# Kernel tuning notes

Hardware: AMD Instinct MI355X
Metric: run time of the kernel (lower is better)

The kernel has to match this reference:

```python
import jax, jax.numpy as jnp
import numpy as np

N = 200000
F = 64   # input_node_features_size
H = 64   # input_node_hidden_state_size
E = 64   # input_edge_hidden_state_size
DEG = 16
OUT = 128          # output_node_hidden_state_size
HALF = OUT // 2    # 64
IN1 = F + H        # 128 (first_layer=False -> concat)
MID1 = (F + H + HALF) // 2  # 96


def setup_inputs() -> dict:
    key = jax.random.key(0)
    ks = jax.random.split(key, 11)
    s = lambda fan_in: 1.0 / np.sqrt(fan_in)
    return {
        "node_features": jax.random.normal(ks[0], (N, F), jnp.float32),
        "node_hidden": jax.random.normal(ks[1], (N, H), jnp.float32),
        "mailbox": jax.random.normal(ks[2], (N, DEG, E), jnp.float32),
        # net_1: Linear(IN1->MID1), Linear(MID1->HALF)
        "w1a": jax.random.uniform(ks[3], (IN1, MID1), jnp.float32, -s(IN1), s(IN1)),
        "b1a": jax.random.uniform(ks[4], (MID1,), jnp.float32, -s(IN1), s(IN1)),
        "w1b": jax.random.uniform(ks[5], (MID1, HALF), jnp.float32, -s(MID1), s(MID1)),
        "b1b": jax.random.uniform(ks[6], (HALF,), jnp.float32, -s(MID1), s(MID1)),
        # net_2: Linear(E->HALF), Linear(HALF->HALF)
        "w2a": jax.random.uniform(ks[7], (E, HALF), jnp.float32, -s(E), s(E)),
        "b2a": jax.random.uniform(ks[8], (HALF,), jnp.float32, -s(E), s(E)),
        "w2b": jax.random.uniform(ks[9], (HALF, HALF), jnp.float32, -s(HALF), s(HALF)),
        "b2b": jax.random.uniform(ks[10], (HALF,), jnp.float32, -s(HALF), s(HALF)),
    }


def reference(node_features, node_hidden, mailbox,
              w1a, b1a, w1b, b1b, w2a, b2a, w2b, b2b):
    # Branch 1: concat(features, hidden) -> Linear -> ReLU -> Linear -> Tanh
    # (dropout is identity at inference)
    x1 = jnp.concatenate([node_features, node_hidden], axis=1)  # [N, IN1]
    h1 = jax.nn.relu(x1 @ w1a + b1a)                            # [N, MID1]
    r1 = jnp.tanh(h1 @ w1b + b1b)                               # [N, HALF]

    # Branch 2: mailbox sum-aggregate -> Linear -> ReLU -> Linear -> Tanh
    x2 = jnp.sum(mailbox, axis=1)                               # [N, E]
    h2 = jax.nn.relu(x2 @ w2a + b2a)                            # [N, HALF]
    r2 = jnp.tanh(h2 @ w2b + b2b)                               # [N, HALF]

    # Concat + per-row L2 (Frobenius over dim=1) normalize
    r = jnp.concatenate([r1, r2], axis=1)                       # [N, OUT]
    norm = jnp.linalg.norm(r, axis=1, keepdims=True)
    return r / norm
```

## Files before the change

kernel.cpp:

```cpp
#include <hip/hip_runtime.h>

constexpr int NB = 64;
constexpr int THREADS = 256;
constexpr int X1SU = 66;
constexpr int H1SU = 50;
constexpr int X2SU = 35;

constexpr int W1A_OFF = 0;
constexpr int W1B_OFF = 6144;
constexpr int W2A_OFF = 9216;
constexpr int W2B_OFF = 11264;
constexpr int WTOTAL  = 13312;

typedef __fp16 half2_t __attribute__((ext_vector_type(2)));

__device__ __forceinline__ float fast_tanh(float x) {
    float e = __expf(2.0f * x);
    return 1.0f - 2.0f * __builtin_amdgcn_rcpf(e + 1.0f);
}

__device__ __forceinline__ unsigned pk16(float a, float b) {
    half2_t h = __builtin_amdgcn_cvt_pkrtz(a, b);
    return __builtin_bit_cast(unsigned, h);
}

__device__ __forceinline__ half2_t uh(unsigned u) {
    return __builtin_bit_cast(half2_t, u);
}

__device__ __forceinline__ void dot24(half2_t pa, half2_t pb,
                                      const unsigned* __restrict__ w0,
                                      const unsigned* __restrict__ w1,
                                      float* __restrict__ acc) {
    #pragma unroll
    for (int j = 0; j < 24; ++j) acc[j] = __builtin_amdgcn_fdot2(pa, uh(w0[j]), acc[j], false);
    #pragma unroll
    for (int j = 0; j < 24; ++j) acc[j] = __builtin_amdgcn_fdot2(pb, uh(w1[j]), acc[j], false);
}

__device__ __forceinline__ void dot16(half2_t pa, half2_t pb,
                                      const unsigned* __restrict__ w0,
                                      const unsigned* __restrict__ w1,
                                      float* __restrict__ acc) {
    #pragma unroll
    for (int j = 0; j < 16; ++j) acc[j] = __builtin_amdgcn_fdot2(pa, uh(w0[j]), acc[j], false);
    #pragma unroll
    for (int j = 0; j < 16; ++j) acc[j] = __builtin_amdgcn_fdot2(pb, uh(w1[j]), acc[j], false);
}

__global__ __launch_bounds__(256) void cvt_weights(
    const float* __restrict__ w1a, const float* __restrict__ w1b,
    const float* __restrict__ w2a, const float* __restrict__ w2b,
    unsigned* __restrict__ wp)
{
    int idx = blockIdx.x * 256 + threadIdx.x;
    const float* src; int cols, rel;
    if (idx < W1B_OFF)      { rel = idx;           src = w1a; cols = 96; }
    else if (idx < W2A_OFF) { rel = idx - W1B_OFF; src = w1b; cols = 64; }
    else if (idx < W2B_OFF) { rel = idx - W2A_OFF; src = w2a; cols = 64; }
    else                    { rel = idx - W2B_OFF; src = w2b; cols = 64; }
    int k2 = rel / cols, j = rel - k2 * cols;
    wp[idx] = pk16(src[(2 * k2) * cols + j], src[(2 * k2 + 1) * cols + j]);
}

__global__ __launch_bounds__(THREADS) void node_net_kernel(
    const float* __restrict__ feat, const float* __restrict__ hid,
    const float* __restrict__ mail,
    const float* __restrict__ b1a, const float* __restrict__ b1b,
    const float* __restrict__ b2a, const float* __restrict__ b2b,
    const unsigned* __restrict__ wp,
    float* __restrict__ out)
{
    __shared__ unsigned ldsA[NB * X1SU];
    __shared__ unsigned ldsB[NB * X2SU];
    __shared__ float    ldsS[NB * 4];

    const int t  = threadIdx.x;
    const int n0 = blockIdx.x * NB;
    const int c4 = t & 15;
    const int nb = t >> 4;

    const float4* mb0 = reinterpret_cast<const float4*>(mail) + (size_t)(n0 + nb) * 256 + c4;

    #pragma unroll
    for (int i = 0; i < 4; ++i) {
        int n = nb + 16 * i;
        float4 f = reinterpret_cast<const float4*>(feat)[(size_t)(n0 + n) * 16 + c4];
        float4 g = reinterpret_cast<const float4*>(hid )[(size_t)(n0 + n) * 16 + c4];
        unsigned* dst = &ldsA[n * X1SU];
        *reinterpret_cast<uint2*>(dst + c4 * 2)      = make_uint2(pk16(f.x, f.y), pk16(f.z, f.w));
        *reinterpret_cast<uint2*>(dst + 32 + c4 * 2) = make_uint2(pk16(g.x, g.y), pk16(g.z, g.w));
    }
    __syncthreads();

    const int node = t & 63;
    const int sub  = __builtin_amdgcn_readfirstlane(t >> 6);

    float acc1[24];
    {
        const float* b = b1a + sub * 24;
        #pragma unroll
        for (int j = 0; j < 24; ++j) acc1[j] = b[j];
    }
    {
        const unsigned* xr = &ldsA[node * X1SU];
        const unsigned* w1aP = wp + W1A_OFF + sub * 24;
        #pragma unroll 1
        for (int c = 0; c < 4; ++c) {
            const float4* chain = mb0 + (size_t)c * 4096;
            float4 m;
            #pragma unroll
            for (int half = 0; half < 2; ++half) {
                float4 cur[8];
                #pragma unroll
                for (int d = 0; d < 8; ++d)
                    cur[d] = chain[(half * 8 + d) * 16];
                __builtin_amdgcn_sched_barrier(0);
                #pragma unroll
                for (int kk = 0; kk < 4; ++kk) {
                    int k4 = (c * 2 + half) * 4 + kk;
                    uint2 xu = *reinterpret_cast<const uint2*>(xr + 2 * k4);
                    dot24(uh(xu.x), uh(xu.y),
                          w1aP + (2 * k4) * 96, w1aP + (2 * k4 + 1) * 96, acc1);
                }
                __builtin_amdgcn_sched_barrier(0);
                float4 s = ((cur[0] + cur[1]) + (cur[2] + cur[3]))
                         + ((cur[4] + cur[5]) + (cur[6] + cur[7]));
                if (half == 0) m = s; else m += s;
            }
            *reinterpret_cast<uint2*>(&ldsB[(nb + 16 * c) * X2SU + c4 * 2]) =
                make_uint2(pk16(m.x, m.y), pk16(m.z, m.w));
        }
    }
    __syncthreads();
    {
        unsigned* hv = &ldsA[node * H1SU + sub * 12];
        #pragma unroll
        for (int p = 0; p < 12; ++p)
            hv[p] = pk16(fmaxf(acc1[2*p], 0.f), fmaxf(acc1[2*p + 1], 0.f));
    }
    __syncthreads();

    float r1v[16];
    {
        float acc[16];
        const float* b = b1b + sub * 16;
        #pragma unroll
        for (int j = 0; j < 16; ++j) acc[j] = b[j];
        const unsigned* hb = &ldsA[node * H1SU];
        const unsigned* w1bP = wp + W1B_OFF + sub * 16;
        #pragma unroll 2
        for (int k4 = 0; k4 < 24; ++k4) {
            uint2 hu2 = *reinterpret_cast<const uint2*>(hb + 2 * k4);
            dot16(uh(hu2.x), uh(hu2.y),
                  w1bP + (2 * k4) * 64, w1bP + (2 * k4 + 1) * 64, acc);
        }
        #pragma unroll
        for (int j = 0; j < 16; ++j) r1v[j] = fast_tanh(acc[j]);
    }

    float h2v[16];
    {
        float acc[16];
        const float* b = b2a + sub * 16;
        #pragma unroll
        for (int j = 0; j < 16; ++j) acc[j] = b[j];
        const unsigned* xb = &ldsB[node * X2SU];
        const unsigned* w2aP = wp + W2A_OFF + sub * 16;
        #pragma unroll 2
        for (int k4 = 0; k4 < 16; ++k4) {
            uint2 xu = *reinterpret_cast<const uint2*>(xb + 2 * k4);
            dot16(uh(xu.x), uh(xu.y),
                  w2aP + (2 * k4) * 64, w2aP + (2 * k4 + 1) * 64, acc);
        }
        #pragma unroll
        for (int j = 0; j < 16; ++j) h2v[j] = fmaxf(acc[j], 0.f);
    }
    __syncthreads();
    {
        unsigned* hrow = &ldsB[node * X2SU + sub * 8];
        #pragma unroll
        for (int p = 0; p < 8; ++p)
            hrow[p] = pk16(h2v[2*p], h2v[2*p + 1]);
    }
    __syncthreads();

    float r2v[16];
    {
        float acc[16];
        const float* b = b2b + sub * 16;
        #pragma unroll
        for (int j = 0; j < 16; ++j) acc[j] = b[j];
        const unsigned* hb2 = &ldsB[node * X2SU];
        const unsigned* w2bP = wp + W2B_OFF + sub * 16;
        #pragma unroll 2
        for (int k4 = 0; k4 < 16; ++k4) {
            uint2 xu = *reinterpret_cast<const uint2*>(hb2 + 2 * k4);
            dot16(uh(xu.x), uh(xu.y),
                  w2bP + (2 * k4) * 64, w2bP + (2 * k4 + 1) * 64, acc);
        }
        #pragma unroll
        for (int j = 0; j < 16; ++j) r2v[j] = fast_tanh(acc[j]);
    }

    float s = 0.f;
    #pragma unroll
    for (int j = 0; j < 16; ++j) s = fmaf(r1v[j], r1v[j], s);
    #pragma unroll
    for (int j = 0; j < 16; ++j) s = fmaf(r2v[j], r2v[j], s);
    ldsS[node * 4 + sub] = s;
    __syncthreads();
    float4 sv = reinterpret_cast<const float4*>(ldsS)[node];
    float rn = rsqrtf(sv.x + sv.y + sv.z + sv.w);

    float* orow = out + (size_t)(n0 + node) * 128;
    float4* o1 = reinterpret_cast<float4*>(orow + sub * 16);
    float4* o2 = reinterpret_cast<float4*>(orow + 64 + sub * 16);
    #pragma unroll
    for (int j4 = 0; j4 < 4; ++j4) {
        o1[j4] = make_float4(r1v[j4*4+0]*rn, r1v[j4*4+1]*rn, r1v[j4*4+2]*rn, r1v[j4*4+3]*rn);
        o2[j4] = make_float4(r2v[j4*4+0]*rn, r2v[j4*4+1]*rn, r2v[j4*4+2]*rn, r2v[j4*4+3]*rn);
    }
}

extern "C" void kernel_launch(void* const* d_in, const int* in_sizes, int n_in,
                              void* d_out, int out_size, void* d_ws, size_t ws_size,
                              hipStream_t stream) {
    const float* feat = (const float*)d_in[0];
    const float* hid  = (const float*)d_in[1];
    const float* mail = (const float*)d_in[2];
    const float* w1a  = (const float*)d_in[3];
    const float* b1a  = (const float*)d_in[4];
    const float* w1b  = (const float*)d_in[5];
    const float* b1b  = (const float*)d_in[6];
    const float* w2a  = (const float*)d_in[7];
    const float* b2a  = (const float*)d_in[8];
    const float* w2b  = (const float*)d_in[9];
    const float* b2b  = (const float*)d_in[10];
    float* out = (float*)d_out;
    unsigned* wp = (unsigned*)d_ws;

    const int N = in_sizes[0] / 64;
    const int blocks = N / NB;

    cvt_weights<<<WTOTAL / 256, 256, 0, stream>>>(w1a, w1b, w2a, w2b, wp);
    node_net_kernel<<<blocks, THREADS, 0, stream>>>(
        feat, hid, mail, b1a, b1b, b2a, b2b, wp, out);
}
```

Before: 232.0 us.

## Reassign mailbox loads so each wave streams whole nodes contiguously

Changes the mailbox aggregation so each wave reads two full contiguous 4 KB node mailboxes per iteration, instead of each thread striding across 16 nodes. Partial sums are combined with cross-lane xor shuffles, and lanes 0-31 write the two reduced rows to LDS. The aim is fully contiguous, better-coalesced global loads per wave and fewer outstanding registers. The cost is added shuffle work and lane-divergent stores, and the loop now has 8 iterations with 8 loads each, which changes how much load latency the dot products can hide.

```diff
diff --git a/kernel.cpp b/kernel.cpp
--- a/kernel.cpp
+++ b/kernel.cpp
@@ -26,6 +26,14 @@
 
 __device__ __forceinline__ half2_t uh(unsigned u) {
     return __builtin_bit_cast(half2_t, u);
+}
+
+__device__ __forceinline__ float4 xor_reduce16_32(float4 v) {
+    v.x += __shfl_xor(v.x, 16); v.y += __shfl_xor(v.y, 16);
+    v.z += __shfl_xor(v.z, 16); v.w += __shfl_xor(v.w, 16);
+    v.x += __shfl_xor(v.x, 32); v.y += __shfl_xor(v.y, 32);
+    v.z += __shfl_xor(v.z, 32); v.w += __shfl_xor(v.w, 32);
+    return v;
 }
 
 __device__ __forceinline__ void dot24(half2_t pa, half2_t pb,
@@ -80,8 +88,6 @@
     const int c4 = t & 15;
     const int nb = t >> 4;
 
-    const float4* mb0 = reinterpret_cast<const float4*>(mail) + (size_t)(n0 + nb) * 256 + c4;
-
     #pragma unroll
     for (int i = 0; i < 4; ++i) {
         int n = nb + 16 * i;
@@ -94,6 +100,7 @@
     __syncthreads();
 
     const int node = t & 63;
+    const int l    = t & 63;
     const int sub  = __builtin_amdgcn_readfirstlane(t >> 6);
 
     float acc1[24];
@@ -105,31 +112,32 @@
     {
         const unsigned* xr = &ldsA[node * X1SU];
         const unsigned* w1aP = wp + W1A_OFF + sub * 24;
+        const float4* wbase = reinterpret_cast<const float4*>(mail)
+                            + ((size_t)n0 + sub * 16) * 256;
         #pragma unroll 1
-        for (int c = 0; c < 4; ++c) {
-            const float4* chain = mb0 + (size_t)c * 4096;
-            float4 m;
+        for (int b = 0; b < 8; ++b) {
+            const float4* pA = wbase + (size_t)(2 * b) * 256;
+            const float4* pB = pA + 256;
+            float4 a0 = pA[l], a1 = pA[64 + l], a2 = pA[128 + l], a3 = pA[192 + l];
+            float4 e0 = pB[l], e1 = pB[64 + l], e2 = pB[128 + l], e3 = pB[192 + l];
+            __builtin_amdgcn_sched_barrier(0);
             #pragma unroll
-            for (int half = 0; half < 2; ++half) {
-                float4 cur[8];
-                #pragma unroll
-                for (int d = 0; d < 8; ++d)
-                    cur[d] = chain[(half * 8 + d) * 16];
-                __builtin_amdgcn_sched_barrier(0);
-                #pragma unroll
-                for (int kk = 0; kk < 4; ++kk) {
-                    int k4 = (c * 2 + half) * 4 + kk;
-                    uint2 xu = *reinterpret_cast<const uint2*>(xr + 2 * k4);
-                    dot24(uh(xu.x), uh(xu.y),
-                          w1aP + (2 * k4) * 96, w1aP + (2 * k4 + 1) * 96, acc1);
-                }
-                __builtin_amdgcn_sched_barrier(0);
-                float4 s = ((cur[0] + cur[1]) + (cur[2] + cur[3]))
-                         + ((cur[4] + cur[5]) + (cur[6] + cur[7]));
-                if (half == 0) m = s; else m += s;
+            for (int kk = 0; kk < 4; ++kk) {
+                int k4 = b * 4 + kk;
+                uint2 xu = *reinterpret_cast<const uint2*>(xr + 2 * k4);
+                dot24(uh(xu.x), uh(xu.y),
+                      w1aP + (2 * k4) * 96, w1aP + (2 * k4 + 1) * 96, acc1);
             }
-            *reinterpret_cast<uint2*>(&ldsB[(nb + 16 * c) * X2SU + c4 * 2]) =
-                make_uint2(pk16(m.x, m.y), pk16(m.z, m.w));
+            __builtin_amdgcn_sched_barrier(0);
+            float4 sA = xor_reduce16_32((a0 + a1) + (a2 + a3));
+            float4 sB = xor_reduce16_32((e0 + e1) + (e2 + e3));
+            int nA = sub * 16 + 2 * b;
+            if (l < 16)
+                *reinterpret_cast<uint2*>(&ldsB[nA * X2SU + l * 2]) =
+                    make_uint2(pk16(sA.x, sA.y), pk16(sA.z, sA.w));
+            else if (l < 32)
+                *reinterpret_cast<uint2*>(&ldsB[(nA + 1) * X2SU + (l - 16) * 2]) =
+                    make_uint2(pk16(sB.x, sB.y), pk16(sB.z, sB.w));
         }
     }
     __syncthreads();
```

New measurement: 243.4 us. +4.9%, slower.

## Split mailbox sum-reduction into a separate streaming kernel before the MLP kernel

Applied to the files above, without the earlier changes.

Adds a dedicated kernel that streams the large mailbox tensor, sums over degree and writes a packed fp16 aggregate into workspace. The MLP kernel then reads this small aggregate instead of the raw mailbox. The fused kernel is kept as a fallback when the workspace is too small. The aim is to let the bandwidth-bound reduction run at full occupancy, decoupled from the LDS- and register-heavy MLP. The cost is an extra launch and an extra write and read of the aggregate.

```diff
diff --git a/kernel.cpp b/kernel.cpp
--- a/kernel.cpp
+++ b/kernel.cpp
@@ -63,7 +63,166 @@
     wp[idx] = pk16(src[(2 * k2) * cols + j], src[(2 * k2 + 1) * cols + j]);
 }
 
-__global__ __launch_bounds__(THREADS) void node_net_kernel(
+__global__ __launch_bounds__(256) void mail_reduce(
+    const float* __restrict__ mail, unsigned* __restrict__ x2p)
+{
+    const int t  = threadIdx.x;
+    const int c4 = t & 15;
+    const int nb = t >> 4;
+    const size_t n0 = (size_t)blockIdx.x * NB;
+    #pragma unroll 1
+    for (int i = 0; i < 4; ++i) {
+        const size_t node = n0 + nb + 16 * i;
+        const float4* p = reinterpret_cast<const float4*>(mail) + node * 256 + c4;
+        float4 v[16];
+        #pragma unroll
+        for (int d = 0; d < 16; ++d)
+            v[d] = p[d * 16];
+        float4 s = (((v[0] + v[1]) + (v[2] + v[3])) + ((v[4] + v[5]) + (v[6] + v[7])))
+                 + (((v[8] + v[9]) + (v[10] + v[11])) + ((v[12] + v[13]) + (v[14] + v[15])));
+        reinterpret_cast<uint2*>(x2p)[node * 16 + c4] = make_uint2(pk16(s.x, s.y), pk16(s.z, s.w));
+    }
+}
+
+__global__ __launch_bounds__(THREADS) void node_net_split(
+    const float* __restrict__ feat, const float* __restrict__ hid,
+    const unsigned* __restrict__ x2p,
+    const float* __restrict__ b1a, const float* __restrict__ b1b,
+    const float* __restrict__ b2a, const float* __restrict__ b2b,
+    const unsigned* __restrict__ wp,
+    float* __restrict__ out)
+{
+    __shared__ unsigned ldsA[NB * X1SU];
+    __shared__ unsigned ldsB[NB * X2SU];
+    __shared__ float    ldsS[NB * 4];
+
+    const int t  = threadIdx.x;
+    const int n0 = blockIdx.x * NB;
+    const int c4 = t & 15;
+    const int nb = t >> 4;
+
+    #pragma unroll
+    for (int i = 0; i < 4; ++i) {
+        int n = nb + 16 * i;
+        float4 f = reinterpret_cast<const float4*>(feat)[(size_t)(n0 + n) * 16 + c4];
+        float4 g = reinterpret_cast<const float4*>(hid )[(size_t)(n0 + n) * 16 + c4];
+        uint2  x = reinterpret_cast<const uint2*>(x2p)[(size_t)(n0 + n) * 16 + c4];
+        unsigned* dst = &ldsA[n * X1SU];
+        *reinterpret_cast<uint2*>(dst + c4 * 2)      = make_uint2(pk16(f.x, f.y), pk16(f.z, f.w));
+        *reinterpret_cast<uint2*>(dst + 32 + c4 * 2) = make_uint2(pk16(g.x, g.y), pk16(g.z, g.w));
+        *reinterpret_cast<uint2*>(&ldsB[n * X2SU + c4 * 2]) = x;
+    }
+    __syncthreads();
+
+    const int node = t & 63;
+    const int sub  = __builtin_amdgcn_readfirstlane(t >> 6);
+
+    float acc1[24];
+    {
+        const float* b = b1a + sub * 24;
+        #pragma unroll
+        for (int j = 0; j < 24; ++j) acc1[j] = b[j];
+        const unsigned* xr = &ldsA[node * X1SU];
+        const unsigned* w1aP = wp + W1A_OFF + sub * 24;
+        #pragma unroll 4
+        for (int k4 = 0; k4 < 32; ++k4) {
+            uint2 xu = *reinterpret_cast<const uint2*>(xr + 2 * k4);
+            dot24(uh(xu.x), uh(xu.y),
+                  w1aP + (2 * k4) * 96, w1aP + (2 * k4 + 1) * 96, acc1);
+        }
+    }
+    __syncthreads();
+    {
+        unsigned* hv = &ldsA[node * H1SU + sub * 12];
+        #pragma unroll
+        for (int p = 0; p < 12; ++p)
+            hv[p] = pk16(fmaxf(acc1[2*p], 0.f), fmaxf(acc1[2*p + 1], 0.f));
+    }
+    __syncthreads();
+
+    float r1v[16];
+    {
+        float acc[16];
+        const float* b = b1b + sub * 16;
+        #pragma unroll
+        for (int j = 0; j < 16; ++j) acc[j] = b[j];
+        const unsigned* hb = &ldsA[node * H1SU];
+        const unsigned* w1bP = wp + W1B_OFF + sub * 16;
+        #pragma unroll 2
+        for (int k4 = 0; k4 < 24; ++k4) {
+            uint2 hu2 = *reinterpret_cast<const uint2*>(hb + 2 * k4);
+            dot16(uh(hu2.x), uh(hu2.y),
+                  w1bP + (2 * k4) * 64, w1bP + (2 * k4 + 1) * 64, acc);
+        }
+        #pragma unroll
+        for (int j = 0; j < 16; ++j) r1v[j] = fast_tanh(acc[j]);
+    }
+
+    float h2v[16];
+    {
+        float acc[16];
+        const float* b = b2a + sub * 16;
+        #pragma unroll
+        for (int j = 0; j < 16; ++j) acc[j] = b[j];
+        const unsigned* xb = &ldsB[node * X2SU];
+        const unsigned* w2aP = wp + W2A_OFF + sub * 16;
+        #pragma unroll 2
+        for (int k4 = 0; k4 < 16; ++k4) {
+            uint2 xu = *reinterpret_cast<const uint2*>(xb + 2 * k4);
+            dot16(uh(xu.x), uh(xu.y),
+                  w2aP + (2 * k4) * 64, w2aP + (2 * k4 + 1) * 64, acc);
+        }
+        #pragma unroll
+        for (int j = 0; j < 16; ++j) h2v[j] = fmaxf(acc[j], 0.f);
+    }
+    __syncthreads();
+    {
+        unsigned* hrow = &ldsB[node * X2SU + sub * 8];
+        #pragma unroll
+        for (int p = 0; p < 8; ++p)
+            hrow[p] = pk16(h2v[2*p], h2v[2*p + 1]);
+    }
+    __syncthreads();
+
+    float r2v[16];
+    {
+        float acc[16];
+        const float* b = b2b + sub * 16;
+        #pragma unroll
+        for (int j = 0; j < 16; ++j) acc[j] = b[j];
+        const unsigned* hb2 = &ldsB[node * X2SU];
+        const unsigned* w2bP = wp + W2B_OFF + sub * 16;
+        #pragma unroll 2
+        for (int k4 = 0; k4 < 16; ++k4) {
+            uint2 xu = *reinterpret_cast<const uint2*>(hb2 + 2 * k4);
+            dot16(uh(xu.x), uh(xu.y),
+                  w2bP + (2 * k4) * 64, w2bP + (2 * k4 + 1) * 64, acc);
+        }
+        #pragma unroll
+        for (int j = 0; j < 16; ++j) r2v[j] = fast_tanh(acc[j]);
+    }
+
+    float s = 0.f;
+    #pragma unroll
+    for (int j = 0; j < 16; ++j) s = fmaf(r1v[j], r1v[j], s);
+    #pragma unroll
+    for (int j = 0; j < 16; ++j) s = fmaf(r2v[j], r2v[j], s);
+    ldsS[node * 4 + sub] = s;
+    __syncthreads();
+    float4 sv = reinterpret_cast<const float4*>(ldsS)[node];
+    float rn = rsqrtf(sv.x + sv.y + sv.z + sv.w);
+
+    float* orow = out + (size_t)(n0 + node) * 128;
+    float4* o1 = reinterpret_cast<float4*>(orow + sub * 16);
+    float4* o2 = reinterpret_cast<float4*>(orow + 64 + sub * 16);
+    #pragma unroll
+    for (int j4 = 0; j4 < 4; ++j4) {
+        o1[j4] = make_float4(r1v[j4*4+0]*rn, r1v[j4*4+1]*rn, r1v[j4*4+2]*rn, r1v[j4*4+3]*rn);
+        o2[j4] = make_float4(r2v[j4*4+0]*rn, r2v[j4*4+1]*rn, r2v[j4*4+2]*rn, r2v[j4*4+3]*rn);
+    }
+}
+
+__global__ __launch_bounds__(THREADS) void node_net_fused(
     const float* __restrict__ feat, const float* __restrict__ hid,
     const float* __restrict__ mail,
     const float* __restrict__ b1a, const float* __restrict__ b1b,
@@ -79,7 +238,6 @@
     const int n0 = blockIdx.x * NB;
     const int c4 = t & 15;
     const int nb = t >> 4;
-
     const float4* mb0 = reinterpret_cast<const float4*>(mail) + (size_t)(n0 + nb) * 256 + c4;
 
     #pragma unroll
@@ -244,6 +402,15 @@
     const int blocks = N / NB;
 
     cvt_weights<<<WTOTAL / 256, 256, 0, stream>>>(w1a, w1b, w2a, w2b, wp);
-    node_net_kernel<<<blocks, THREADS, 0, stream>>>(
-        feat, hid, mail, b1a, b1b, b2a, b2b, wp, out);
-}
+
+    const size_t need = (size_t)WTOTAL * 4 + (size_t)N * 128;
+    if (ws_size >= need) {
+        unsigned* x2p = wp + WTOTAL;
+        mail_reduce<<<blocks, 256, 0, stream>>>(mail, x2p);
+        node_net_split<<<blocks, THREADS, 0, stream>>>(
+            feat, hid, x2p, b1a, b1b, b2a, b2b, wp, out);
+    } else {
+        node_net_fused<<<blocks, THREADS, 0, stream>>>(
+            feat, hid, mail, b1a, b1b, b2a, b2b, wp, out);
+    }
+}
```

Result: slower. 288.5 us (+24.4%).
